# Kernel optimization log

Hardware: AMD Instinct MI355X
Metric: run time of the kernel (lower is better)

## Reference

```python
import jax, jax.numpy as jnp
import numpy as np

N, C, H, W = 10, 512, 40, 40
HW = H * W
OUT_CH = 128
EPS = 1e-12

def _l2norm(x, axis):
    # matches F.normalize: v / max(||v||_2, eps)
    n = jnp.sqrt(jnp.sum(x * x, axis=axis, keepdims=True))
    return x / jnp.maximum(n, EPS)

def _conv(x, w, b, pad):
    y = jax.lax.conv_general_dilated(
        x, w, window_strides=(1, 1), padding=[(pad, pad), (pad, pad)],
        dimension_numbers=('NCHW', 'OIHW', 'NCHW'))
    return y + b[None, :, None, None]

def setup_inputs() -> dict:
    key = jax.random.key(0)
    ks = jax.random.split(key, 6)
    feats = jax.random.normal(ks[0], (N, C, H, W), jnp.float32)
    SISMs = jax.random.uniform(ks[1], (N, 1, H, W), jnp.float32)
    # ResNetBlock(HW -> 128) params (Kaiming-uniform-ish fan-in bounds)
    s1 = float(1.0 / np.sqrt(HW * 9))
    s2 = float(1.0 / np.sqrt(OUT_CH * 9))
    ss = float(1.0 / np.sqrt(HW))
    w1 = jax.random.uniform(ks[2], (OUT_CH, HW, 3, 3), jnp.float32, -s1, s1)
    b1 = jnp.zeros((OUT_CH,), jnp.float32)
    w2 = jax.random.uniform(ks[3], (OUT_CH, OUT_CH, 3, 3), jnp.float32, -s2, s2)
    b2 = jnp.zeros((OUT_CH,), jnp.float32)
    ws = jax.random.uniform(ks[4], (OUT_CH, HW, 1, 1), jnp.float32, -ss, ss)
    bs = jnp.zeros((OUT_CH,), jnp.float32)
    return dict(feats=feats, SISMs=SISMs, w1=w1, b1=b1, w2=w2, b2=b2, ws=ws, bs=bs)

def reference(feats, SISMs, w1, b1, w2, b2, ws, bs):
    # SISMs supplied at (H,W): bilinear resize w/ align_corners=True at same size is identity
    NFs = _l2norm(feats, axis=1)                                   # (N,C,H,W)
    SIVs = _l2norm(jnp.mean(NFs * SISMs, axis=(-1, -2)), axis=1)   # (N,C)
    # CFM: 1x1 conv of NFs with SIVs as filters -> (N,N,H,W)
    cm = jnp.einsum('nchw,mc->nmhw', NFs, SIVs).reshape(N, N, HW)
    cm = _l2norm(cm, axis=2)
    corr = jnp.einsum('nmk,npk->nmp', cm, cm)                      # (N,N,N)
    wv = jax.nn.softmax(jnp.sum(corr, axis=2), axis=1)             # (N,N)
    CSA = jnp.sum(cm * wv[:, :, None], axis=1)                     # (N,HW)
    mn = jnp.min(CSA, axis=1, keepdims=True)
    mx = jnp.max(CSA, axis=1, keepdims=True)
    CSA = (CSA - mn) / (mx - mn + EPS)
    CSA_maps = CSA.reshape(N, 1, H, W)
    # self-correlation features: (N, HW, H, W)
    NFf = NFs.reshape(N, C, HW)
    SCFs = jnp.einsum('nci,ncj->nij', NFf, NFf).reshape(N, HW, H, W)
    # reorder channels by descending CSA evidence
    idx = jnp.argsort(-CSA, axis=1)                                # (N,HW)
    RSCFs = jnp.take_along_axis(SCFs, idx[:, :, None, None], axis=1)
    x = RSCFs * CSA_maps
    # ResNetBlock: relu(conv2(relu(conv1(x))) + shortcut_1x1(x))
    h = jax.nn.relu(_conv(x, w1, b1, 1))
    h = _conv(h, w2, b2, 1)
    sc = _conv(x, ws, bs, 0)
    return jax.nn.relu(h + sc)
```

## Files before the change

### kernel.cpp

```cpp
#include <hip/hip_runtime.h>
#include <hip/hip_bf16.h>
#include <math.h>

typedef short short8 __attribute__((ext_vector_type(8)));
typedef short short4v __attribute__((ext_vector_type(4)));
typedef float f32x4 __attribute__((ext_vector_type(4)));
typedef __hip_bfloat16 bf16;

#define KN 10
#define KC 512
#define KHW 1600
#define KH 40
#define KOC 128
#define KPW 42
#define KM 1280

__device__ __forceinline__ void gload16(const void* g, void* l) {
  __builtin_amdgcn_global_load_lds(
      (const __attribute__((address_space(1))) unsigned int*)g,
      (__attribute__((address_space(3))) unsigned int*)l, 16, 0, 0);
}

__device__ __forceinline__ double blockReduceSumD(double v) {
  __shared__ double tmpS[8];
  int lane = threadIdx.x & 63, wv = threadIdx.x >> 6;
  #pragma unroll
  for (int o = 32; o > 0; o >>= 1) v += __shfl_down(v, o);
  if (lane == 0) tmpS[wv] = v;
  __syncthreads();
  if (threadIdx.x == 0) {
    int nw = (blockDim.x + 63) >> 6;
    double s = 0;
    for (int i = 0; i < nw; i++) s += tmpS[i];
    tmpS[0] = s;
  }
  __syncthreads();
  double r = tmpS[0];
  __syncthreads();
  return r;
}

__device__ __forceinline__ double blockReduceMinD(double v) {
  __shared__ double tmpMn[8];
  int lane = threadIdx.x & 63, wv = threadIdx.x >> 6;
  #pragma unroll
  for (int o = 32; o > 0; o >>= 1) v = fmin(v, __shfl_down(v, o));
  if (lane == 0) tmpMn[wv] = v;
  __syncthreads();
  if (threadIdx.x == 0) {
    int nw = (blockDim.x + 63) >> 6;
    double s = tmpMn[0];
    for (int i = 1; i < nw; i++) s = fmin(s, tmpMn[i]);
    tmpMn[0] = s;
  }
  __syncthreads();
  double r = tmpMn[0];
  __syncthreads();
  return r;
}

__device__ __forceinline__ double blockReduceMaxD(double v) {
  __shared__ double tmpMx[8];
  int lane = threadIdx.x & 63, wv = threadIdx.x >> 6;
  #pragma unroll
  for (int o = 32; o > 0; o >>= 1) v = fmax(v, __shfl_down(v, o));
  if (lane == 0) tmpMx[wv] = v;
  __syncthreads();
  if (threadIdx.x == 0) {
    int nw = (blockDim.x + 63) >> 6;
    double s = tmpMx[0];
    for (int i = 1; i < nw; i++) s = fmax(s, tmpMx[i]);
    tmpMx[0] = s;
  }
  __syncthreads();
  double r = tmpMx[0];
  __syncthreads();
  return r;
}


__global__ void k_rnormp(const float* __restrict__ feats, double* __restrict__ ps) {
  int t = blockIdx.x * 256 + threadIdx.x;
  if (t >= KN * KHW) return;
  int ci = blockIdx.y;
  int n = t / KHW, k = t % KHW;
  const float* p = feats + (size_t)n * KC * KHW + (size_t)ci * 32 * KHW + k;
  double s = 0.0;
  #pragma unroll
  for (int c = 0; c < 32; ++c) { double v = p[(size_t)c * KHW]; s += v * v; }
  ps[(size_t)ci * KN * KHW + t] = s;
}

__global__ void k_rnormc(const double* __restrict__ ps, double* __restrict__ rnorm) {
  int t = blockIdx.x * 256 + threadIdx.x;
  if (t >= KN * KHW) return;
  double s = 0;
  #pragma unroll
  for (int ci = 0; ci < 16; ci++) s += ps[(size_t)ci * KN * KHW + t];
  double nn = sqrt(s);
  if (nn < 1e-12) nn = 1e-12;
  rnorm[t] = 1.0 / nn;
}

__global__ void k_nft(const float* __restrict__ feats, const double* __restrict__ rnorm,
                      const float* __restrict__ sism, bf16* __restrict__ NFT,
                      double* __restrict__ vpp) {
  __shared__ float T[32][33];
  int n = blockIdx.z, k0 = blockIdx.x * 32, c0 = blockIdx.y * 32;
  int tx = threadIdx.x, ty = threadIdx.y;
  const float* fb = feats + ((size_t)n * KC + c0) * KHW + k0;
  #pragma unroll
  for (int ii = 0; ii < 4; ii++) {
    int cl = ty * 4 + ii;
    T[cl][tx] = fb[(size_t)cl * KHW + tx];
  }
  __syncthreads();
  bf16* ob = NFT + ((size_t)n * KHW + k0) * KC + c0;
  #pragma unroll
  for (int ii = 0; ii < 4; ii++) {
    int kl = ty * 4 + ii;
    float r = (float)rnorm[n * KHW + k0 + kl];
    ob[(size_t)kl * KC + tx] = __float2bfloat16(T[tx][kl] * r);
  }
  double rs = rnorm[n * KHW + k0 + tx] * (double)sism[n * KHW + k0 + tx];
  #pragma unroll
  for (int ii = 0; ii < 4; ii++) {
    int cl = ty * 4 + ii;
    double v = (double)T[cl][tx] * rs;
    #pragma unroll
    for (int o = 16; o > 0; o >>= 1) v += __shfl_down(v, o, 32);
    if (tx == 0) vpp[((size_t)n * KC + c0 + cl) * 50 + k0 / 32] = v;
  }
}

__global__ void k_sivnorm2(const double* __restrict__ vpp, double* __restrict__ SIV) {
  int n = blockIdx.x, c = threadIdx.x;
  const double* p = vpp + ((size_t)n * KC + c) * 50;
  double acc = 0;
  #pragma unroll 5
  for (int j = 0; j < 50; j++) acc += p[j];
  acc /= (double)KHW;
  double s2 = blockReduceSumD(acc * acc);
  double nn = sqrt(s2);
  if (nn < 1e-12) nn = 1e-12;
  SIV[n * KC + c] = acc / nn;
}

__global__ void k_cmP(const float* __restrict__ feats, const double* __restrict__ SIV,
                      double* __restrict__ cmp) {
  __shared__ double sv[KN][32];
  int kc = blockIdx.x, ci = blockIdx.y, n = blockIdx.z;
  for (int t = threadIdx.x; t < KN * 32; t += 256) {
    int m = t / 32, c = t % 32;
    sv[m][c] = SIV[m * KC + ci * 32 + c];
  }
  __syncthreads();
  int k = kc * 256 + threadIdx.x;
  if (k >= KHW) return;
  const float* f = feats + ((size_t)n * KC + ci * 32) * KHW + k;
  double acc[KN];
  #pragma unroll
  for (int m = 0; m < KN; m++) acc[m] = 0.0;
  for (int c = 0; c < 32; ++c) {
    double fv = f[(size_t)c * KHW];
    #pragma unroll
    for (int m = 0; m < KN; m++) acc[m] += fv * sv[m][c];
  }
  const size_t str = (size_t)KN * KN * KHW;
  #pragma unroll
  for (int m = 0; m < KN; m++)
    cmp[(size_t)ci * str + ((size_t)n * KN + m) * KHW + k] = acc[m];
}

__global__ void k_cmBN(const double* __restrict__ cmp, const double* __restrict__ rnorm,
                       double* __restrict__ cm) {
  int b = blockIdx.x;
  int n = b / KN;
  const size_t str = (size_t)KN * KN * KHW;
  const size_t rb = (size_t)b * KHW;
  double v[4];
  int cnt = 0;
  double ss = 0;
  for (int k = threadIdx.x; k < KHW; k += 512) {
    double s = 0;
    #pragma unroll
    for (int ci = 0; ci < 16; ci++) s += cmp[ci * str + rb + k];
    s *= rnorm[n * KHW + k];
    v[cnt++] = s;
    ss += s * s;
  }
  ss = blockReduceSumD(ss);
  double nn = sqrt(ss);
  if (nn < 1e-12) nn = 1e-12;
  double rn = 1.0 / nn;
  cnt = 0;
  for (int k = threadIdx.x; k < KHW; k += 512) cm[rb + k] = v[cnt++] * rn;
}

__global__ void k_st(const double* __restrict__ cm, double* __restrict__ tbuf) {
  int b = blockIdx.x;
  int n = b / KN, m = b % KN;
  const double* base = cm + (size_t)n * KN * KHW;
  double acc = 0;
  for (int k = threadIdx.x; k < KHW; k += 256) {
    double S = 0;
    #pragma unroll
    for (int mm = 0; mm < KN; mm++) S += base[(size_t)mm * KHW + k];
    acc += base[(size_t)m * KHW + k] * S;
  }
  acc = blockReduceSumD(acc);
  if (threadIdx.x == 0) tbuf[b] = acc;
}

__global__ void k_csa(const double* __restrict__ cm, const double* __restrict__ tbuf,
                      double* __restrict__ CSAd, float* __restrict__ CSAf) {
  __shared__ double w[KN];
  int n = blockIdx.x, tid = threadIdx.x;
  if (tid == 0) {
    double v[KN], mx = -1e300;
    #pragma unroll
    for (int m = 0; m < KN; m++) { v[m] = tbuf[n * KN + m]; mx = fmax(mx, v[m]); }
    double s = 0;
    #pragma unroll
    for (int m = 0; m < KN; m++) { v[m] = exp(v[m] - mx); s += v[m]; }
    #pragma unroll
    for (int m = 0; m < KN; m++) w[m] = v[m] / s;
  }
  __syncthreads();
  double v[7];
  int cnt = 0;
  double lmin = 1e300, lmax = -1e300;
  for (int k = tid; k < KHW; k += 256) {
    double a = 0;
    #pragma unroll
    for (int m = 0; m < KN; m++) a += cm[((size_t)n * KN + m) * KHW + k] * w[m];
    v[cnt++] = a;
    lmin = fmin(lmin, a);
    lmax = fmax(lmax, a);
  }
  double mn = blockReduceMinD(lmin);
  double mx = blockReduceMaxD(lmax);
  double inv = 1.0 / (mx - mn + 1e-12);
  cnt = 0;
  for (int k = tid; k < KHW; k += 256) {
    double nv = (v[cnt++] - mn) * inv;
    CSAd[(size_t)n * KHW + k] = nv;
    CSAf[(size_t)n * KHW + k] = (float)nv;
  }
}

__global__ void k_rank(const double* __restrict__ CSAd, int* __restrict__ idx) {
  __shared__ double key[KHW];
  int b = blockIdx.x;
  int n = b / 100, it = b % 100;
  const double* src = CSAd + (size_t)n * KHW;
  for (int j = threadIdx.x; j < KHW; j += 256) key[j] = src[j];
  __syncthreads();
  int wave = threadIdx.x >> 6, lane = threadIdx.x & 63;
  int i0 = it * 16 + wave * 4;
  double ki[4];
  #pragma unroll
  for (int ii = 0; ii < 4; ii++) ki[ii] = key[i0 + ii];
  int r[4] = {0, 0, 0, 0};
  #pragma unroll
  for (int q = 0; q < 25; q++) {
    int j = q * 64 + lane;
    double kj = key[j];
    #pragma unroll
    for (int ii = 0; ii < 4; ii++) {
      int i = i0 + ii;
      r[ii] += (kj > ki[ii]) || (kj == ki[ii] && j < i);
    }
  }
  #pragma unroll
  for (int ii = 0; ii < 4; ii++) {
    int v = r[ii];
    #pragma unroll
    for (int o = 32; o > 0; o >>= 1) v += __shfl_down(v, o);
    if (lane == 0) idx[n * KHW + v] = i0 + ii;
  }
}

__global__ void k_prepw1s(const float* __restrict__ w1, const float* __restrict__ wsc,
                          bf16* __restrict__ w1s) {
  int t = blockIdx.x * 256 + threadIdx.x;
  int m = t / KHW, i = t % KHW;
  int tau = m >> 7, o = m & 127;
  float v = (tau < 9) ? w1[((size_t)o * KHW + i) * 9 + tau]
                      : wsc[(size_t)o * KHW + i];
  w1s[t] = __float2bfloat16(v);
}

__global__ void k_prepw2(const float* __restrict__ w2, bf16* __restrict__ w2p) {
  int t = blockIdx.x * 256 + threadIdx.x;
  if (t >= KOC * 9 * KOC) return;
  int o = t / (9 * KOC), r = t % (9 * KOC);
  int s = r / KOC, i = r % KOC;
  w2p[t] = __float2bfloat16(w2[(size_t)o * 9 * KOC + (size_t)i * 9 + s]);
}

__global__ void k_zborder(bf16* __restrict__ Zpad, bf16* __restrict__ hpadT) {
  int t = blockIdx.x * 256 + threadIdx.x;
  const int ZW = KN * 164 * (KC / 8);
  const int HWm = KN * 164 * (KOC / 8);
  int b;
  if (t < ZW) {
    int n = t / (164 * 64), r = t % (164 * 64);
    b = r / 64;
    int c8 = r % 64;
    int y, x;
    if (b < 42) { y = 0; x = b; }
    else if (b < 84) { y = 41; x = b - 42; }
    else if (b < 124) { y = b - 84 + 1; x = 0; }
    else { y = b - 124 + 1; x = 41; }
    short8 z = {};
    *(short8*)((short*)Zpad + ((size_t)n * KPW * KPW + (size_t)y * KPW + x) * KC + c8 * 8) = z;
  } else if (t < ZW + HWm) {
    int u = t - ZW;
    int n = u / (164 * 16), r = u % (164 * 16);
    b = r / 16;
    int c8 = r % 16;
    int y, x;
    if (b < 42) { y = 0; x = b; }
    else if (b < 84) { y = 41; x = b - 42; }
    else if (b < 124) { y = b - 84 + 1; x = 0; }
    else { y = b - 124 + 1; x = 41; }
    short8 z = {};
    *(short8*)((short*)hpadT + ((size_t)n * KPW * KPW + (size_t)y * KPW + x) * KOC + c8 * 8) = z;
  }
}

__global__ void k_gath2(const short* __restrict__ NFT, const int* __restrict__ idx,
                        short* __restrict__ NFcg) {
  __shared__ short T[32][33];
  int i0 = blockIdx.x * 32, c0 = blockIdx.y * 32, n = blockIdx.z;
  int tx = threadIdx.x, ty = threadIdx.y;
  #pragma unroll
  for (int ii = 0; ii < 4; ii++) {
    int row = ty * 4 + ii;
    int id = idx[n * KHW + i0 + row];
    T[row][tx] = NFT[((size_t)n * KHW + id) * KC + c0 + tx];
  }
  __syncthreads();
  #pragma unroll
  for (int ii = 0; ii < 4; ii++) {
    int cl = ty * 4 + ii;
    NFcg[((size_t)n * KC + c0 + cl) * KHW + i0 + tx] = T[tx][cl];
  }
}

__global__ void k_zprep(const bf16* __restrict__ NFT, const float* __restrict__ CSAf,
                        bf16* __restrict__ Zpad) {
  int t = blockIdx.x * 256 + threadIdx.x;
  const int per_n = KHW * (KC / 4);
  int n = t / per_n, r = t % per_n;
  int p = r / (KC / 4), cq = r % (KC / 4);
  float cs = CSAf[n * KHW + p];
  const short* src = (const short*)(NFT + ((size_t)n * KHW + p) * KC) + cq * 4;
  short4v v = *(const short4v*)src;
  short4v o;
  #pragma unroll
  for (int j = 0; j < 4; j++) {
    short s = v[j];
    bf16 hb = *reinterpret_cast<bf16*>(&s);
    bf16 res = __float2bfloat16(__bfloat162float(hb) * cs);
    o[j] = *reinterpret_cast<short*>(&res);
  }
  int y = p / KH, x = p % KH;
  short* dst = (short*)(Zpad + ((size_t)n * KPW * KPW + (size_t)(y + 1) * KPW + (x + 1)) * KC) + cq * 4;
  *(short4v*)dst = o;
}

__global__ __launch_bounds__(256) void k_gemmU(const short* __restrict__ w1s,
                                               const short* __restrict__ NFcg,
                                               bf16* __restrict__ Uc,
                                               bf16* __restrict__ Usc) {
  __shared__ __align__(16) short smem[24576];
  short* As = smem;
  short* Bs = smem + 8192;
  short* Cs = smem;
  int b = blockIdx.x;
  int workid = (b & 7) * 100 + (b >> 3);
  int pair = workid / 20;
  int th = workid % 20;
  int n = pair >> 2, c0 = (pair & 3) * 128;
  int tau = th >> 1, half = th & 1;
  int m0 = tau * 128 + half * 64;
  int tid = threadIdx.x, lane = tid & 63, wave = tid >> 6;
  int quad = lane >> 4, l15 = lane & 15;
  int wm = (wave & 1) * 32, wn = (wave >> 1) * 64;
  int sk = ((tid & 7) ^ ((tid >> 3) & 7)) * 8;
  int rowg = tid >> 3;
  const short* Bb = NFcg + (size_t)n * KC * KHW;
  const short* pA[2];
  #pragma unroll
  for (int g = 0; g < 2; g++)
    pA[g] = w1s + (size_t)(m0 + g * 32 + rowg) * KHW + sk;
  const short* pB[4];
  #pragma unroll
  for (int g = 0; g < 4; g++)
    pB[g] = Bb + (size_t)(c0 + g * 32 + rowg) * KHW + sk;
  char* lA = (char*)As + tid * 16;
  char* lB = (char*)Bs + tid * 16;
  int bq = (l15 >> 2) & 1;
  int qx = (quad ^ (l15 & 3)) * 8;
  int koff0 = 32 * bq + qx;
  int koff1 = 32 * (1 - bq) + qx;
  f32x4 acc[2][4] = {};
  gload16(pA[0], lA); gload16(pA[1], lA + 4096);
  gload16(pB[0], lB); gload16(pB[1], lB + 4096);
  gload16(pB[2], lB + 8192); gload16(pB[3], lB + 12288);
  __syncthreads();
  const int NS = 25;
  for (int s = 0; s < NS; s++) {
    int cb = s & 1, nb = cb ^ 1;
    if (s + 1 < NS) {
      int off = (s + 1) * 64;
      char* la = lA + nb * 8192;
      char* lb = lB + nb * 16384;
      gload16(pA[0] + off, la); gload16(pA[1] + off, la + 4096);
      gload16(pB[0] + off, lb); gload16(pB[1] + off, lb + 4096);
      gload16(pB[2] + off, lb + 8192); gload16(pB[3] + off, lb + 12288);
    }
    const short* Ab = As + cb * 4096;
    const short* Bbf = Bs + cb * 8192;
    #pragma unroll
    for (int ks = 0; ks < 2; ks++) {
      int ko = (ks == 0) ? koff0 : koff1;
      short8 av[2], bv[4];
      #pragma unroll
      for (int t = 0; t < 2; t++) av[t] = *(const short8*)&Ab[(wm + t * 16 + l15) * 64 + ko];
      #pragma unroll
      for (int t = 0; t < 4; t++) bv[t] = *(const short8*)&Bbf[(wn + t * 16 + l15) * 64 + ko];
      #pragma unroll
      for (int ti = 0; ti < 2; ti++)
        #pragma unroll
        for (int tj = 0; tj < 4; tj++)
          acc[ti][tj] = __builtin_amdgcn_mfma_f32_16x16x32_bf16(av[ti], bv[tj], acc[ti][tj], 0, 0, 0);
    }
    __syncthreads();
  }
  #pragma unroll
  for (int ti = 0; ti < 2; ti++) {
    int lr = wm + ti * 16 + quad * 4;
    #pragma unroll
    for (int tj = 0; tj < 4; tj++) {
      int lc = wn + tj * 16 + l15;
      #pragma unroll
      for (int r = 0; r < 4; r++)
        *(bf16*)&Cs[(lr + r) * 136 + lc] = __float2bfloat16(acc[ti][tj][r]);
    }
  }
  __syncthreads();
  int dyq = tau / 3, dxq = tau % 3;
  #pragma unroll
  for (int pass = 0; pass < 4; pass++) {
    int row = pass * 16 + (tid >> 4);
    int col = (tid & 15) * 8;
    if (tau < 9) {
      *(float4*)&Uc[((size_t)((n * 3 + dyq) * 128 + half * 64 + row)) * 1536 + dxq * 512 + c0 + col] =
          *(const float4*)&Cs[row * 136 + col];
    } else {
      *(float4*)&Usc[((size_t)(n * 128 + half * 64 + row)) * 512 + c0 + col] =
          *(const float4*)&Cs[row * 136 + col];
    }
  }
}

__global__ __launch_bounds__(256) void k_convh(const short* __restrict__ Uc,
                                               const short* __restrict__ Usc,
                                               const short* __restrict__ Zpad,
                                               float* __restrict__ Hpart) {
  __shared__ __align__(16) short smem[24576];
  short* As = smem;
  short* Bs = smem + 16384;
  int b = blockIdx.x;
  int wgid = (b & 7) * 125 + (b >> 3);
  int n = wgid / 100, rest = wgid % 100;
  int dy = rest / 25, pt = rest % 25;
  int p0 = pt * 64;
  int tid = threadIdx.x, lane = tid & 63, wave = tid >> 6;
  int quad = lane >> 4, l15 = lane & 15;
  int wm = (wave & 1) * 64, wn = (wave >> 1) * 32;
  int sk = ((tid & 7) ^ ((tid >> 3) & 7)) * 8;
  int rowg = tid >> 3;
  bool isconv = (dy < 3);
  const short* Zb = Zpad + (size_t)n * KPW * KPW * KC;
  const short* Abase = isconv ? Uc + ((size_t)((n * 3 + dy) * 128)) * 1536
                              : Usc + ((size_t)(n * 128)) * 512;
  int astr = isconv ? 1536 : 512;
  const short* pA[4];
  #pragma unroll
  for (int g = 0; g < 4; g++)
    pA[g] = Abase + (size_t)(g * 32 + rowg) * astr + sk;
  const short* pB[2];
  #pragma unroll
  for (int g = 0; g < 2; g++) {
    int p = p0 + g * 32 + rowg;
    int y = p / KH, x = p % KH;
    int yy = isconv ? (y + dy) : (y + 1);
    int xx = isconv ? x : (x + 1);
    pB[g] = Zb + ((size_t)yy * KPW + xx) * KC + sk;
  }
  char* lA = (char*)As + tid * 16;
  char* lB = (char*)Bs + tid * 16;
  int NS = isconv ? 24 : 8;
  int bq = (l15 >> 2) & 1;
  int qx = (quad ^ (l15 & 3)) * 8;
  int koff0 = 32 * bq + qx;
  int koff1 = 32 * (1 - bq) + qx;
  f32x4 acc[4][2] = {};
  gload16(pA[0], lA); gload16(pA[1], lA + 4096);
  gload16(pA[2], lA + 8192); gload16(pA[3], lA + 12288);
  gload16(pB[0], lB); gload16(pB[1], lB + 4096);
  __syncthreads();
  for (int s = 0; s < NS; s++) {
    int cb = s & 1, nb = cb ^ 1;
    if (s + 1 < NS) {
      int off = (s + 1) * 64;
      char* la = lA + nb * 16384;
      char* lb = lB + nb * 8192;
      gload16(pA[0] + off, la); gload16(pA[1] + off, la + 4096);
      gload16(pA[2] + off, la + 8192); gload16(pA[3] + off, la + 12288);
      gload16(pB[0] + off, lb); gload16(pB[1] + off, lb + 4096);
    }
    const short* Ab = As + cb * 8192;
    const short* Bb = Bs + cb * 4096;
    #pragma unroll
    for (int ks = 0; ks < 2; ks++) {
      int ko = (ks == 0) ? koff0 : koff1;
      short8 av[4], bv[2];
      #pragma unroll
      for (int t = 0; t < 4; t++) av[t] = *(const short8*)&Ab[(wm + t * 16 + l15) * 64 + ko];
      #pragma unroll
      for (int t = 0; t < 2; t++) bv[t] = *(const short8*)&Bb[(wn + t * 16 + l15) * 64 + ko];
      #pragma unroll
      for (int ti = 0; ti < 4; ti++)
        #pragma unroll
        for (int tj = 0; tj < 2; tj++)
          acc[ti][tj] = __builtin_amdgcn_mfma_f32_16x16x32_bf16(av[ti], bv[tj], acc[ti][tj], 0, 0, 0);
    }
    __syncthreads();
  }
  float* cbp = Hpart + ((size_t)(dy * KN + n)) * KOC * KHW;
  #pragma unroll
  for (int ti = 0; ti < 4; ti++) {
    int o = wm + ti * 16 + quad * 4;
    #pragma unroll
    for (int tj = 0; tj < 2; tj++) {
      int q = p0 + wn + tj * 16 + l15;
      #pragma unroll
      for (int r = 0; r < 4; r++)
        cbp[(size_t)(o + r) * KHW + q] = acc[ti][tj][r];
    }
  }
}

__global__ void k_hprep3(const float* __restrict__ Hpart, const float* __restrict__ b1,
                         bf16* __restrict__ hpadT) {
  __shared__ float T[32][132];
  int n = blockIdx.y, p0 = blockIdx.x * 32;
  int tx = threadIdx.x, ty = threadIdx.y;
  const size_t str = (size_t)KN * KOC * KHW;
  const float* hb = Hpart + (size_t)n * KOC * KHW;
  #pragma unroll
  for (int oc = 0; oc < 16; oc++) {
    int o = oc * 8 + ty;
    size_t off = (size_t)o * KHW + p0 + tx;
    T[tx][o] = fmaxf(hb[off] + hb[str + off] + hb[2 * str + off] + b1[o], 0.0f);
  }
  __syncthreads();
  bf16* hp = hpadT + (size_t)n * KPW * KPW * KOC;
  #pragma unroll
  for (int pc = 0; pc < 4; pc++) {
    int pl = ty * 4 + pc;
    int pp = p0 + pl;
    int yy = pp / KH, xx = pp % KH;
    bf16* row = hp + ((size_t)(yy + 1) * KPW + (xx + 1)) * KOC;
    #pragma unroll
    for (int u = 0; u < 4; u++) row[tx * 4 + u] = __float2bfloat16(T[pl][tx * 4 + u]);
  }
}

__global__ __launch_bounds__(256) void k_conv2(const short* __restrict__ w2p,
                                               const short* __restrict__ hpadT,
                                               float* __restrict__ Cpart) {
  __shared__ __align__(16) short smem[24576];
  short* As = smem;
  short* Bs = smem + 16384;
  int b = blockIdx.x;
  int xcd = b & 7, bi = b >> 3;
  int wgid = (xcd < 6 ? xcd * 94 : 6 * 94 + (xcd - 6) * 93) + bi;
  int n = wgid / 75, rest = wgid % 75;
  int dy = rest / 25, pt = rest % 25;
  int p0 = pt * 64;
  int tid = threadIdx.x, lane = tid & 63, wave = tid >> 6;
  int quad = lane >> 4, l15 = lane & 15;
  int wm = (wave & 1) * 64, wn = (wave >> 1) * 32;
  int sk = ((tid & 7) ^ ((tid >> 3) & 7)) * 8;
  int rowg = tid >> 3;
  const short* hb = hpadT + (size_t)n * KPW * KPW * KOC;
  const short* pA[4];
  #pragma unroll
  for (int g = 0; g < 4; g++)
    pA[g] = w2p + (size_t)(g * 32 + rowg) * (9 * KOC) + dy * 384 + sk;
  const short* pB[2];
  #pragma unroll
  for (int g = 0; g < 2; g++) {
    int p = p0 + g * 32 + rowg;
    int y = p / KH, x = p % KH;
    pB[g] = hb + ((size_t)(y + dy) * KPW + x) * KOC + sk;
  }
  char* lA = (char*)As + tid * 16;
  char* lB = (char*)Bs + tid * 16;
  const int NS = 6;
  int bq = (l15 >> 2) & 1;
  int qx = (quad ^ (l15 & 3)) * 8;
  int koff0 = 32 * bq + qx;
  int koff1 = 32 * (1 - bq) + qx;
  f32x4 acc[4][2] = {};
  gload16(pA[0], lA); gload16(pA[1], lA + 4096);
  gload16(pA[2], lA + 8192); gload16(pA[3], lA + 12288);
  gload16(pB[0], lB); gload16(pB[1], lB + 4096);
  __syncthreads();
  for (int s = 0; s < NS; s++) {
    int cb = s & 1, nb = cb ^ 1;
    if (s + 1 < NS) {
      int off = (s + 1) * 64;
      char* la = lA + nb * 16384;
      char* lb = lB + nb * 8192;
      gload16(pA[0] + off, la); gload16(pA[1] + off, la + 4096);
      gload16(pA[2] + off, la + 8192); gload16(pA[3] + off, la + 12288);
      gload16(pB[0] + off, lb); gload16(pB[1] + off, lb + 4096);
    }
    const short* Ab = As + cb * 8192;
    const short* Bb = Bs + cb * 4096;
    #pragma unroll
    for (int ks = 0; ks < 2; ks++) {
      int ko = (ks == 0) ? koff0 : koff1;
      short8 av[4], bv[2];
      #pragma unroll
      for (int t = 0; t < 4; t++) av[t] = *(const short8*)&Ab[(wm + t * 16 + l15) * 64 + ko];
      #pragma unroll
      for (int t = 0; t < 2; t++) bv[t] = *(const short8*)&Bb[(wn + t * 16 + l15) * 64 + ko];
      #pragma unroll
      for (int ti = 0; ti < 4; ti++)
        #pragma unroll
        for (int tj = 0; tj < 2; tj++)
          acc[ti][tj] = __builtin_amdgcn_mfma_f32_16x16x32_bf16(av[ti], bv[tj], acc[ti][tj], 0, 0, 0);
    }
    __syncthreads();
  }
  float* cbp = Cpart + ((size_t)(dy * KN + n)) * KOC * KHW;
  #pragma unroll
  for (int ti = 0; ti < 4; ti++) {
    int o = wm + ti * 16 + quad * 4;
    #pragma unroll
    for (int tj = 0; tj < 2; tj++) {
      int q = p0 + wn + tj * 16 + l15;
      #pragma unroll
      for (int r = 0; r < 4; r++)
        cbp[(size_t)(o + r) * KHW + q] = acc[ti][tj][r];
    }
  }
}

__global__ void k_final2(const float* __restrict__ Cpart, const float* __restrict__ Hpart,
                         const float* __restrict__ b2, const float* __restrict__ bs,
                         float* __restrict__ out) {
  int t = blockIdx.x * 256 + threadIdx.x;
  if (t >= KN * KOC * KHW) return;
  int o = (t / KHW) % KOC;
  const size_t stride = (size_t)KN * KOC * KHW;
  float v = Cpart[t] + Cpart[stride + t] + Cpart[2 * stride + t] +
            Hpart[3 * stride + t] + b2[o] + bs[o];
  out[t] = fmaxf(v, 0.0f);
}

extern "C" void kernel_launch(void* const* d_in, const int* in_sizes, int n_in,
                              void* d_out, int out_size, void* d_ws, size_t ws_size,
                              hipStream_t stream) {
  const float* feats = (const float*)d_in[0];
  const float* sisms = (const float*)d_in[1];
  const float* w1 = (const float*)d_in[2];
  const float* b1 = (const float*)d_in[3];
  const float* w2 = (const float*)d_in[4];
  const float* b2 = (const float*)d_in[5];
  const float* wsc = (const float*)d_in[6];
  const float* bsc = (const float*)d_in[7];
  float* out = (float*)d_out;

  char* w = (char*)d_ws;
  auto carve = [&](size_t bytes) -> void* {
    void* p = (void*)w;
    w += (bytes + 255) & ~(size_t)255;
    return p;
  };
  bf16* NFT   = (bf16*)carve((size_t)KN * KHW * KC * 2);
  bf16* NFcg  = (bf16*)carve((size_t)KN * KC * KHW * 2);
  bf16* Uc    = (bf16*)carve((size_t)KN * 3 * 128 * 1536 * 2);
  bf16* Usc   = (bf16*)carve((size_t)KN * 128 * 512 * 2);
  bf16* w1s   = (bf16*)carve((size_t)KM * KHW * 2);
  bf16* Zpad  = (bf16*)carve((size_t)KN * KPW * KPW * KC * 2);
  bf16* hpadT = (bf16*)carve((size_t)KN * KPW * KPW * KOC * 2);
  float* Hpart = (float*)carve((size_t)4 * KN * KOC * KHW * 4);
  float* Cpart = (float*)carve((size_t)3 * KN * KOC * KHW * 4);
  bf16* w2p   = (bf16*)carve((size_t)KOC * 9 * KOC * 2);
  double* psbuf = (double*)carve((size_t)16 * KN * KHW * 8);
  double* rnorm = (double*)carve((size_t)KN * KHW * 8);
  double* vpp   = (double*)carve((size_t)KN * KC * 50 * 8);
  double* SIV   = (double*)carve((size_t)KN * KC * 8);
  double* cmp   = (double*)carve((size_t)16 * KN * KN * KHW * 8);
  double* cm    = (double*)carve((size_t)KN * KN * KHW * 8);
  double* tbuf  = (double*)carve((size_t)KN * KN * 8);
  double* CSAd  = (double*)carve((size_t)KN * KHW * 8);
  float* CSAf   = (float*)carve((size_t)KN * KHW * 4);
  int* idxb     = (int*)carve((size_t)KN * KHW * 4);

  k_zborder<<<513, 256, 0, stream>>>(Zpad, hpadT);

  k_rnormp<<<dim3(63, 16), 256, 0, stream>>>(feats, psbuf);
  k_rnormc<<<63, 256, 0, stream>>>(psbuf, rnorm);
  k_nft<<<dim3(50, 16, KN), dim3(32, 8), 0, stream>>>(feats, rnorm, sisms, NFT, vpp);
  k_sivnorm2<<<KN, 512, 0, stream>>>(vpp, SIV);
  k_cmP<<<dim3(7, 16, KN), 256, 0, stream>>>(feats, SIV, cmp);
  k_cmBN<<<KN * KN, 512, 0, stream>>>(cmp, rnorm, cm);
  k_st<<<KN * KN, 256, 0, stream>>>(cm, tbuf);
  k_csa<<<KN, 256, 0, stream>>>(cm, tbuf, CSAd, CSAf);
  k_rank<<<1000, 256, 0, stream>>>(CSAd, idxb);

  k_prepw1s<<<KM * KHW / 256, 256, 0, stream>>>(w1, wsc, w1s);
  k_prepw2<<<576, 256, 0, stream>>>(w2, w2p);
  k_gath2<<<dim3(50, 16, KN), dim3(32, 8), 0, stream>>>((const short*)NFT, idxb, (short*)NFcg);
  k_zprep<<<KN * KHW * (KC / 4) / 256, 256, 0, stream>>>(NFT, CSAf, Zpad);

  k_gemmU<<<800, 256, 0, stream>>>((const short*)w1s, (const short*)NFcg, Uc, Usc);
  k_convh<<<1000, 256, 0, stream>>>((const short*)Uc, (const short*)Usc,
                                    (const short*)Zpad, Hpart);
  k_hprep3<<<dim3(50, KN), dim3(32, 8), 0, stream>>>(Hpart, b1, hpadT);
  k_conv2<<<750, 256, 0, stream>>>((const short*)w2p, (const short*)hpadT, Cpart);
  k_final2<<<8000, 256, 0, stream>>>(Cpart, Hpart, b2, bsc, out);
}
```

Baseline: 275.0 us.

## Fuse conv2 dy split-K and final epilogue into single kernel; remap convh blocks

The conv2 kernel no longer splits the 3x3 reduction across dy into three partial buffers. Each block now loops over all 18 K-steps (3 dy × 3 dx × 2 halves) for a 128x32 tile and applies bias, the shortcut add and ReLU directly, so the Cpart buffer and the separate k_final2 pass are gone. This removes a large fp32 partial write/read round trip and one launch. The cost is a longer serial K loop per block, fewer blocks (500), and narrower N tiles with lower MFMA reuse. Separately, k_convh's block-to-work mapping puts the conv blocks first with XCD-balanced ordering and the shortcut blocks after them.

```diff
diff --git a/kernel.cpp b/kernel.cpp
--- a/kernel.cpp
+++ b/kernel.cpp
@@ -475,16 +475,24 @@
   short* As = smem;
   short* Bs = smem + 16384;
   int b = blockIdx.x;
-  int wgid = (b & 7) * 125 + (b >> 3);
-  int n = wgid / 100, rest = wgid % 100;
-  int dy = rest / 25, pt = rest % 25;
+  bool isconv = (b < 750);
+  int n, dy, pt;
+  if (isconv) {
+    int xcd = b & 7, bi = b >> 3;
+    int wgid = (xcd < 6 ? xcd * 94 : 6 * 94 + (xcd - 6) * 93) + bi;
+    n = wgid / 75;
+    int rest = wgid % 75;
+    dy = rest / 25; pt = rest % 25;
+  } else {
+    int u = b - 750;
+    n = u / 25; pt = u % 25; dy = 3;
+  }
   int p0 = pt * 64;
   int tid = threadIdx.x, lane = tid & 63, wave = tid >> 6;
   int quad = lane >> 4, l15 = lane & 15;
   int wm = (wave & 1) * 64, wn = (wave >> 1) * 32;
   int sk = ((tid & 7) ^ ((tid >> 3) & 7)) * 8;
   int rowg = tid >> 3;
-  bool isconv = (dy < 3);
   const short* Zb = Zpad + (size_t)n * KPW * KPW * KC;
   const short* Abase = isconv ? Uc + ((size_t)((n * 3 + dy) * 128)) * 1536
                               : Usc + ((size_t)(n * 128)) * 512;
@@ -582,99 +590,87 @@
   }
 }
 
-__global__ __launch_bounds__(256) void k_conv2(const short* __restrict__ w2p,
-                                               const short* __restrict__ hpadT,
-                                               float* __restrict__ Cpart) {
-  __shared__ __align__(16) short smem[24576];
+__global__ __launch_bounds__(256) void k_conv2f(const short* __restrict__ w2p,
+                                                const short* __restrict__ hpadT,
+                                                const float* __restrict__ Hpart,
+                                                const float* __restrict__ b2,
+                                                const float* __restrict__ bs,
+                                                float* __restrict__ out) {
+  __shared__ __align__(16) short smem[20480];
   short* As = smem;
   short* Bs = smem + 16384;
   int b = blockIdx.x;
   int xcd = b & 7, bi = b >> 3;
-  int wgid = (xcd < 6 ? xcd * 94 : 6 * 94 + (xcd - 6) * 93) + bi;
-  int n = wgid / 75, rest = wgid % 75;
-  int dy = rest / 25, pt = rest % 25;
-  int p0 = pt * 64;
+  int wgid = (xcd < 4 ? xcd * 63 : 4 * 63 + (xcd - 4) * 62) + bi;
+  int n = wgid / 50, pt = wgid % 50;
+  int p0 = pt * 32;
   int tid = threadIdx.x, lane = tid & 63, wave = tid >> 6;
   int quad = lane >> 4, l15 = lane & 15;
-  int wm = (wave & 1) * 64, wn = (wave >> 1) * 32;
+  int wm = (wave & 1) * 64, wn = (wave >> 1) * 16;
   int sk = ((tid & 7) ^ ((tid >> 3) & 7)) * 8;
   int rowg = tid >> 3;
   const short* hb = hpadT + (size_t)n * KPW * KPW * KOC;
   const short* pA[4];
   #pragma unroll
   for (int g = 0; g < 4; g++)
-    pA[g] = w2p + (size_t)(g * 32 + rowg) * (9 * KOC) + dy * 384 + sk;
-  const short* pB[2];
-  #pragma unroll
-  for (int g = 0; g < 2; g++) {
-    int p = p0 + g * 32 + rowg;
-    int y = p / KH, x = p % KH;
-    pB[g] = hb + ((size_t)(y + dy) * KPW + x) * KOC + sk;
-  }
+    pA[g] = w2p + (size_t)(g * 32 + rowg) * (9 * KOC) + sk;
+  int prow = p0 + rowg;
+  int py = prow / KH, px = prow % KH;
+  const short* pB0 = hb + ((size_t)py * KPW + px) * KOC + sk;
   char* lA = (char*)As + tid * 16;
   char* lB = (char*)Bs + tid * 16;
-  const int NS = 6;
   int bq = (l15 >> 2) & 1;
   int qx = (quad ^ (l15 & 3)) * 8;
   int koff0 = 32 * bq + qx;
   int koff1 = 32 * (1 - bq) + qx;
-  f32x4 acc[4][2] = {};
+  f32x4 acc[4] = {};
+  const int NS = 18;
   gload16(pA[0], lA); gload16(pA[1], lA + 4096);
   gload16(pA[2], lA + 8192); gload16(pA[3], lA + 12288);
-  gload16(pB[0], lB); gload16(pB[1], lB + 4096);
+  gload16(pB0, lB);
   __syncthreads();
   for (int s = 0; s < NS; s++) {
     int cb = s & 1, nb = cb ^ 1;
     if (s + 1 < NS) {
-      int off = (s + 1) * 64;
+      int s2 = s + 1;
+      int dy = s2 / 6, dxq = (s2 % 6) >> 1, kh = (s2 & 1) * 64;
+      int ao = (dy * 3 + dxq) * 128 + kh;
+      int bo = (dy * 42 + dxq) * 128 + kh;
       char* la = lA + nb * 16384;
-      char* lb = lB + nb * 8192;
-      gload16(pA[0] + off, la); gload16(pA[1] + off, la + 4096);
-      gload16(pA[2] + off, la + 8192); gload16(pA[3] + off, la + 12288);
-      gload16(pB[0] + off, lb); gload16(pB[1] + off, lb + 4096);
+      char* lb = lB + nb * 4096;
+      gload16(pA[0] + ao, la); gload16(pA[1] + ao, la + 4096);
+      gload16(pA[2] + ao, la + 8192); gload16(pA[3] + ao, la + 12288);
+      gload16(pB0 + bo, lb);
     }
     const short* Ab = As + cb * 8192;
-    const short* Bb = Bs + cb * 4096;
+    const short* Bb = Bs + cb * 2048;
     #pragma unroll
     for (int ks = 0; ks < 2; ks++) {
       int ko = (ks == 0) ? koff0 : koff1;
-      short8 av[4], bv[2];
+      short8 av[4], bv;
       #pragma unroll
       for (int t = 0; t < 4; t++) av[t] = *(const short8*)&Ab[(wm + t * 16 + l15) * 64 + ko];
-      #pragma unroll
-      for (int t = 0; t < 2; t++) bv[t] = *(const short8*)&Bb[(wn + t * 16 + l15) * 64 + ko];
+      bv = *(const short8*)&Bb[(wn + l15) * 64 + ko];
       #pragma unroll
       for (int ti = 0; ti < 4; ti++)
-        #pragma unroll
-        for (int tj = 0; tj < 2; tj++)
-          acc[ti][tj] = __builtin_amdgcn_mfma_f32_16x16x32_bf16(av[ti], bv[tj], acc[ti][tj], 0, 0, 0);
+        acc[ti] = __builtin_amdgcn_mfma_f32_16x16x32_bf16(av[ti], bv, acc[ti], 0, 0, 0);
     }
     __syncthreads();
   }
-  float* cbp = Cpart + ((size_t)(dy * KN + n)) * KOC * KHW;
+  const float* hsc = Hpart + ((size_t)(3 * KN + n)) * KOC * KHW;
+  float* ob = out + (size_t)n * KOC * KHW;
+  int q = p0 + wn + l15;
   #pragma unroll
   for (int ti = 0; ti < 4; ti++) {
     int o = wm + ti * 16 + quad * 4;
-    #pragma unroll
-    for (int tj = 0; tj < 2; tj++) {
-      int q = p0 + wn + tj * 16 + l15;
-      #pragma unroll
-      for (int r = 0; r < 4; r++)
-        cbp[(size_t)(o + r) * KHW + q] = acc[ti][tj][r];
-    }
-  }
-}
-
-__global__ void k_final2(const float* __restrict__ Cpart, const float* __restrict__ Hpart,
-                         const float* __restrict__ b2, const float* __restrict__ bs,
-                         float* __restrict__ out) {
-  int t = blockIdx.x * 256 + threadIdx.x;
-  if (t >= KN * KOC * KHW) return;
-  int o = (t / KHW) % KOC;
-  const size_t stride = (size_t)KN * KOC * KHW;
-  float v = Cpart[t] + Cpart[stride + t] + Cpart[2 * stride + t] +
-            Hpart[3 * stride + t] + b2[o] + bs[o];
-  out[t] = fmaxf(v, 0.0f);
+    f32x4 b2v = *(const f32x4*)&b2[o];
+    f32x4 bsv = *(const f32x4*)&bs[o];
+    #pragma unroll
+    for (int r = 0; r < 4; r++) {
+      float v = acc[ti][r] + b2v[r] + bsv[r] + hsc[(size_t)(o + r) * KHW + q];
+      ob[(size_t)(o + r) * KHW + q] = fmaxf(v, 0.0f);
+    }
+  }
 }
 
 extern "C" void kernel_launch(void* const* d_in, const int* in_sizes, int n_in,
@@ -704,7 +700,6 @@
   bf16* Zpad  = (bf16*)carve((size_t)KN * KPW * KPW * KC * 2);
   bf16* hpadT = (bf16*)carve((size_t)KN * KPW * KPW * KOC * 2);
   float* Hpart = (float*)carve((size_t)4 * KN * KOC * KHW * 4);
-  float* Cpart = (float*)carve((size_t)3 * KN * KOC * KHW * 4);
   bf16* w2p   = (bf16*)carve((size_t)KOC * 9 * KOC * 2);
   double* psbuf = (double*)carve((size_t)16 * KN * KHW * 8);
   double* rnorm = (double*)carve((size_t)KN * KHW * 8);
@@ -738,6 +733,6 @@
   k_convh<<<1000, 256, 0, stream>>>((const short*)Uc, (const short*)Usc,
                                     (const short*)Zpad, Hpart);
   k_hprep3<<<dim3(50, KN), dim3(32, 8), 0, stream>>>(Hpart, b1, hpadT);
-  k_conv2<<<750, 256, 0, stream>>>((const short*)w2p, (const short*)hpadT, Cpart);
-  k_final2<<<8000, 256, 0, stream>>>(Cpart, Hpart, b2, bsc, out);
-}
+  k_conv2f<<<500, 256, 0, stream>>>((const short*)w2p, (const short*)hpadT,
+                                    Hpart, b2, bsc, out);
+}
```

Result: no change. 270.6 us (-1.6%).
